# Performance work log

Hardware: AMD Instinct MI355X
Metric: run time of the kernel (lower is better)

## Reference

```python
import jax, jax.numpy as jnp
import numpy as np

B, C = 2, 2
D = H = W = 192
N_BIF = 64                 # bif ids 0..63; labels = bif*4 + stub (stub in 1..3)
NUM_LABELS = 4 * N_BIF     # 256
MIN_STUBS = 2
MIN_VOXELS = 1
TEMP = 0.2


def setup_inputs() -> dict:
    key = jax.random.key(0)
    k1, k2 = jax.random.split(key)
    pred = jax.random.normal(k1, (B, C, D, H, W), dtype=jnp.float32)
    stub_label_map = jax.random.randint(k2, (B, 1, D, H, W), 0, NUM_LABELS).astype(jnp.float32)
    return {"pred": pred, "stub_label_map": stub_label_map}


def reference(pred, stub_label_map):
    # foreground probability: softmax over channel dim, take class 1
    fg = jax.nn.softmax(pred, axis=1)[:, 1]                     # [B,D,H,W]
    labels = jnp.round(stub_label_map[:, 0]).astype(jnp.int32)  # [B,D,H,W]

    Bn = fg.shape[0]
    fg_flat = fg.reshape(Bn, -1)
    lab_flat = labels.reshape(Bn, -1)

    seg = lambda v, i: jax.ops.segment_sum(v, i, num_segments=NUM_LABELS)
    sums = jax.vmap(seg)(fg_flat, lab_flat)                      # [B, NUM_LABELS]
    counts = jax.vmap(seg)(jnp.ones_like(fg_flat), lab_flat)     # [B, NUM_LABELS]

    # group labels as [bif, stub]; drop bif 0 and stub 0 (never used in loop)
    sums = sums.reshape(Bn, N_BIF, 4)[:, 1:, 1:4]                # [B, N_BIF-1, 3]
    counts = counts.reshape(Bn, N_BIF, 4)[:, 1:, 1:4]

    valid = counts >= MIN_VOXELS                                 # stub has enough voxels
    means = sums / jnp.maximum(counts, 1.0)                      # per-stub mean fg prob

    # softmin over the valid stubs of each bif (masked softmax of -mean/temp)
    logits = jnp.where(valid, -means / TEMP, -1e9)
    weights = jax.nn.softmax(logits, axis=-1)
    score = jnp.sum(jnp.where(valid, means * weights, 0.0), axis=-1)  # [B, N_BIF-1]

    valid_bif = jnp.sum(valid, axis=-1) >= MIN_STUBS
    total = jnp.sum(jnp.where(valid_bif, 1.0 - score, 0.0))
    n_bifs = jnp.sum(valid_bif)
    return jnp.where(n_bifs > 0, total / jnp.maximum(n_bifs, 1).astype(total.dtype), 0.0)
```

## Files before the change

kernel.cpp:

```cpp
#include <hip/hip_runtime.h>
#include <math.h>

#define BATCH     2
#define NLAB      256
#define VOX       (192*192*192)
#define TEMP      0.2f
#define GRIDX     768
#define NITER     (VOX / (GRIDX * 1024))
#define NPART     16

#define STEP      4096.0f
#define INV_STEP  (1.0f/4096.0f)

typedef unsigned int u32;
typedef __attribute__((ext_vector_type(8))) short bf16x8;
typedef __attribute__((ext_vector_type(4))) float f32x4;
union FragU { uint4 u; bf16x8 v; };

__device__ __forceinline__ u32 packvox(float pa, float pc, float pl) {
    const float fg = 1.0f / (1.0f + __expf(pa - pc));
    u32 bits = __float_as_uint(fg);
    bits += 0x7FFFu + ((bits >> 16) & 1u);
    const u32 lab = ((u32)(int)(pl + 0.5f)) & 255u;
    return (lab << 24) | (bits >> 16);
}

#define PAIR(de, dodd, aw, b1w, b2w) do {                                   \
    const u32 _e = (de), _o = (dodd);                                       \
    const bool he  = ((_e >> 28) == mlane);                                 \
    const bool ho  = ((_o >> 28) == mlane);                                 \
    const bool le  = (((_e >> 24) & 15u) == mlane);                         \
    const bool lo_ = (((_o >> 24) & 15u) == mlane);                         \
    aw  = (he ? 0x00003F80u : 0u) | (ho  ? 0x3F800000u : 0u);               \
    b1w = (le ? 0x00003F80u : 0u) | (lo_ ? 0x3F800000u : 0u);               \
    b2w = (le ? (_e & 0xFFFFu) : 0u) | (lo_ ? (_o << 16) : 0u);             \
} while (0)

__global__ __launch_bounds__(256, 4) void histo_kernel(
    const float* __restrict__ pred,
    const float* __restrict__ labmap,
    float* __restrict__ ws_slots)
{
    __shared__ __align__(16) u32 s_stage[4][2][256];
    __shared__ float s_cnt[4][NLAB];
    __shared__ float s_sum[4][NLAB];

    const int b    = blockIdx.y;
    const int tid  = threadIdx.x;
    const int w    = tid >> 6;
    const int lane = tid & 63;
    const u32 mlane = (u32)(lane & 15);
    const int g    = lane >> 4;

    const float4* p0 = (const float4*)(pred + (size_t)b * 2 * VOX);
    const float4* p1 = (const float4*)(pred + (size_t)b * 2 * VOX + VOX);
    const float4* lm = (const float4*)(labmap + (size_t)b * VOX);

    f32x4 accC = {0.f, 0.f, 0.f, 0.f};
    f32x4 accS = {0.f, 0.f, 0.f, 0.f};

    const int base = blockIdx.x * 256 + tid;

    #pragma unroll 2
    for (int it = 0; it < NITER; ++it) {
        const int i = base + it * (GRIDX * 256);
        const float4 a = p0[i];
        const float4 c = p1[i];
        const float4 l = lm[i];

        uint4 pkv;
        pkv.x = packvox(a.x, c.x, l.x);
        pkv.y = packvox(a.y, c.y, l.y);
        pkv.z = packvox(a.z, c.z, l.z);
        pkv.w = packvox(a.w, c.w, l.w);

        u32* st = &s_stage[w][it & 1][0];
        *(uint4*)(st + (lane << 2)) = pkv;

        const u32* rp = st + (g << 3);
        #pragma unroll
        for (int t = 0; t < 8; ++t) {
            const uint4 q0 = *(const uint4*)(rp + t * 32);
            const uint4 q1 = *(const uint4*)(rp + t * 32 + 4);
            u32 a0, a1, a2, a3, b10, b11, b12, b13, b20, b21, b22, b23;
            PAIR(q0.x, q0.y, a0, b10, b20);
            PAIR(q0.z, q0.w, a1, b11, b21);
            PAIR(q1.x, q1.y, a2, b12, b22);
            PAIR(q1.z, q1.w, a3, b13, b23);
            FragU A, B1, B2;
            A.u  = make_uint4(a0, a1, a2, a3);
            B1.u = make_uint4(b10, b11, b12, b13);
            B2.u = make_uint4(b20, b21, b22, b23);
            accC = __builtin_amdgcn_mfma_f32_16x16x32_bf16(A.v, B1.v, accC, 0, 0, 0);
            accS = __builtin_amdgcn_mfma_f32_16x16x32_bf16(A.v, B2.v, accS, 0, 0, 0);
        }
    }

    const int row0 = (lane >> 4) << 2;
    const int colb = lane & 15;
    #pragma unroll
    for (int j = 0; j < 4; ++j) {
        s_cnt[w][(row0 + j) * 16 + colb] = accC[j];
        s_sum[w][(row0 + j) * 16 + colb] = accS[j];
    }
    __syncthreads();

    const float cs = s_cnt[0][tid] + s_cnt[1][tid] + s_cnt[2][tid] + s_cnt[3][tid];
    const float ss = s_sum[0][tid] + s_sum[1][tid] + s_sum[2][tid] + s_sum[3][tid];
    ws_slots[((size_t)(b * GRIDX + blockIdx.x)) * NLAB + tid] = ss + STEP * cs;
}

__global__ __launch_bounds__(256) void reduce_kernel(
    const float* __restrict__ ws_slots,
    float* __restrict__ psum,
    float* __restrict__ pcnt)
{
    const int bin  = threadIdx.x;
    const int b    = blockIdx.x / NPART;
    const int part = blockIdx.x % NPART;
    const int per  = GRIDX / NPART;

    float cs = 0.0f, ss = 0.0f;
    for (int s = part * per; s < (part + 1) * per; ++s) {
        float v = ws_slots[((size_t)(b * GRIDX + s)) * NLAB + bin];
        float c = floorf(v * INV_STEP + 0.5f);
        cs += c;
        ss += v - c * STEP;
    }
    psum[(size_t)blockIdx.x * NLAB + bin] = ss;
    pcnt[(size_t)blockIdx.x * NLAB + bin] = cs;
}

__global__ __launch_bounds__(256) void scalar_kernel(
    const float* __restrict__ psum,
    const float* __restrict__ pcnt,
    float* __restrict__ out)
{
    __shared__ float s_fsum[BATCH][NLAB];
    __shared__ float s_fcnt[BATCH][NLAB];

    const int tid = threadIdx.x;

    for (int b = 0; b < BATCH; ++b) {
        float ss = 0.0f, cs = 0.0f;
        for (int p = 0; p < NPART; ++p) {
            ss += psum[(size_t)(b * NPART + p) * NLAB + tid];
            cs += pcnt[(size_t)(b * NPART + p) * NLAB + tid];
        }
        s_fsum[b][tid] = ss;
        s_fcnt[b][tid] = cs;
    }
    __syncthreads();

    if (tid < 64) {
        float total = 0.0f;
        float nbifs = 0.0f;
        if (tid >= 1) {
            for (int bb = 0; bb < BATCH; ++bb) {
                float means[3];
                bool  valid[3];
                int   nvalid = 0;
                for (int s = 0; s < 3; ++s) {
                    int lab = tid * 4 + 1 + s;
                    float cnt = s_fcnt[bb][lab];
                    float sum = s_fsum[bb][lab];
                    valid[s] = (cnt >= 1.0f);
                    means[s] = sum / fmaxf(cnt, 1.0f);
                    nvalid  += valid[s] ? 1 : 0;
                }
                float logits[3], m = -3e38f;
                for (int s = 0; s < 3; ++s) {
                    logits[s] = valid[s] ? (-means[s] / TEMP) : -1e9f;
                    m = fmaxf(m, logits[s]);
                }
                float e[3], se = 0.0f;
                for (int s = 0; s < 3; ++s) { e[s] = __expf(logits[s] - m); se += e[s]; }
                float score = 0.0f;
                for (int s = 0; s < 3; ++s) {
                    if (valid[s]) score += means[s] * (e[s] / se);
                }
                if (nvalid >= 2) {
                    total += 1.0f - score;
                    nbifs += 1.0f;
                }
            }
        }
        for (int off = 32; off > 0; off >>= 1) {
            total += __shfl_down(total, off);
            nbifs += __shfl_down(nbifs, off);
        }
        if (tid == 0) {
            out[0] = (nbifs > 0.0f) ? (total / fmaxf(nbifs, 1.0f)) : 0.0f;
        }
    }
}

extern "C" void kernel_launch(void* const* d_in, const int* in_sizes, int n_in,
                              void* d_out, int out_size, void* d_ws, size_t ws_size,
                              hipStream_t stream) {
    const float* pred = (const float*)d_in[0];
    const float* lab  = (const float*)d_in[1];

    float* ws_slots = (float*)d_ws;
    float* psum = ws_slots + (size_t)BATCH * GRIDX * NLAB;
    float* pcnt = psum + (size_t)BATCH * NPART * NLAB;

    dim3 grid(GRIDX, BATCH);
    histo_kernel<<<grid, 256, 0, stream>>>(pred, lab, ws_slots);
    reduce_kernel<<<BATCH * NPART, 256, 0, stream>>>(ws_slots, psum, pcnt);
    scalar_kernel<<<1, 256, 0, stream>>>(psum, pcnt, (float*)d_out);
}
```

Measured before the change: 217.1 us.

## Split histogram work between LDS-atomic blocks and MFMA blocks in one kernel

The histogram kernel now assigns 4 of every 9 blocks to an LDS-atomic path, which keeps two interleaved histogram copies and skips unused labels. The other 5 of every 9 blocks keep the MFMA one-hot path. Running both paths side by side balances VALU/LDS-atomic work against matrix-core work, and the grid drops to 576 blocks of 12 iterations each with launch bounds relaxed. This adds divergent code paths per block and depends on the two paths covering exactly the whole voxel range. Atomic contention and the fixed 4:5 ratio may not suit the hardware.

Measured after the change: 224.6 us. 3.5% more time.

```diff
diff --git a/kernel.cpp b/kernel.cpp
--- a/kernel.cpp
+++ b/kernel.cpp
@@ -4,10 +4,14 @@
 #define BATCH     2
 #define NLAB      256
 #define VOX       (192*192*192)
+#define VVEC      (VOX/4)
 #define TEMP      0.2f
-#define GRIDX     768
-#define NITER     (VOX / (GRIDX * 1024))
+
+#define BLOCKS    576
+#define NITER     12
 #define NPART     16
+#define NATOMIC_ORDS 256
+#define MFMA_F4_BASE (NATOMIC_ORDS * NITER * 256)
 
 #define STEP      4096.0f
 #define INV_STEP  (1.0f/4096.0f)
@@ -36,78 +40,127 @@
     b2w = (le ? (_e & 0xFFFFu) : 0u) | (lo_ ? (_o << 16) : 0u);             \
 } while (0)
 
-__global__ __launch_bounds__(256, 4) void histo_kernel(
+__global__ __launch_bounds__(256) void histo_kernel(
     const float* __restrict__ pred,
     const float* __restrict__ labmap,
     float* __restrict__ ws_slots)
 {
-    __shared__ __align__(16) u32 s_stage[4][2][256];
-    __shared__ float s_cnt[4][NLAB];
-    __shared__ float s_sum[4][NLAB];
-
-    const int b    = blockIdx.y;
-    const int tid  = threadIdx.x;
-    const int w    = tid >> 6;
-    const int lane = tid & 63;
-    const u32 mlane = (u32)(lane & 15);
-    const int g    = lane >> 4;
+    __shared__ __align__(16) u32 s_lds[4][2][256];
+
+    const int b   = blockIdx.y;
+    const int bx  = blockIdx.x;
+    const int tid = threadIdx.x;
+    const int j   = bx % 9;
+    const int grp = bx / 9;
 
     const float4* p0 = (const float4*)(pred + (size_t)b * 2 * VOX);
     const float4* p1 = (const float4*)(pred + (size_t)b * 2 * VOX + VOX);
     const float4* lm = (const float4*)(labmap + (size_t)b * VOX);
 
-    f32x4 accC = {0.f, 0.f, 0.f, 0.f};
-    f32x4 accS = {0.f, 0.f, 0.f, 0.f};
-
-    const int base = blockIdx.x * 256 + tid;
-
-    #pragma unroll 2
-    for (int it = 0; it < NITER; ++it) {
-        const int i = base + it * (GRIDX * 256);
-        const float4 a = p0[i];
-        const float4 c = p1[i];
-        const float4 l = lm[i];
-
-        uint4 pkv;
-        pkv.x = packvox(a.x, c.x, l.x);
-        pkv.y = packvox(a.y, c.y, l.y);
-        pkv.z = packvox(a.z, c.z, l.z);
-        pkv.w = packvox(a.w, c.w, l.w);
-
-        u32* st = &s_stage[w][it & 1][0];
-        *(uint4*)(st + (lane << 2)) = pkv;
-
-        const u32* rp = st + (g << 3);
+    float val;
+
+    if (j < 4) {
+        float* h = (float*)&s_lds[0][0][0];
+        h[tid] = 0.0f;
+        h[tid + NLAB] = 0.0f;
+        __syncthreads();
+
+        const int ord  = grp * 4 + j;
+        const int copy = (tid & 1) << 8;
+        const int base = ord * (NITER * 256) + tid;
+
+        #pragma unroll 3
+        for (int it = 0; it < NITER; ++it) {
+            const int i = base + it * 256;
+            const float4 a = p0[i];
+            const float4 c = p1[i];
+            const float4 l = lm[i];
+
+            float fg0 = 1.0f / (1.0f + __expf(a.x - c.x));
+            float fg1 = 1.0f / (1.0f + __expf(a.y - c.y));
+            float fg2 = 1.0f / (1.0f + __expf(a.z - c.z));
+            float fg3 = 1.0f / (1.0f + __expf(a.w - c.w));
+
+            int l0 = ((int)(l.x + 0.5f)) & (NLAB - 1);
+            int l1 = ((int)(l.y + 0.5f)) & (NLAB - 1);
+            int l2 = ((int)(l.z + 0.5f)) & (NLAB - 1);
+            int l3 = ((int)(l.w + 0.5f)) & (NLAB - 1);
+
+            if ((l0 & 3) && l0 >= 4) atomicAdd(&h[copy + l0], STEP + fg0);
+            if ((l1 & 3) && l1 >= 4) atomicAdd(&h[copy + l1], STEP + fg1);
+            if ((l2 & 3) && l2 >= 4) atomicAdd(&h[copy + l2], STEP + fg2);
+            if ((l3 & 3) && l3 >= 4) atomicAdd(&h[copy + l3], STEP + fg3);
+        }
+        __syncthreads();
+        val = h[tid] + h[tid + NLAB];
+    } else {
+        const int w    = tid >> 6;
+        const int lane = tid & 63;
+        const u32 mlane = (u32)(lane & 15);
+        const int g    = lane >> 4;
+
+        f32x4 accC = {0.f, 0.f, 0.f, 0.f};
+        f32x4 accS = {0.f, 0.f, 0.f, 0.f};
+
+        const int ord  = grp * 5 + (j - 4);
+        const int base = MFMA_F4_BASE + ord * (NITER * 256) + tid;
+
+        #pragma unroll 2
+        for (int it = 0; it < NITER; ++it) {
+            const int i = base + it * 256;
+            const float4 a = p0[i];
+            const float4 c = p1[i];
+            const float4 l = lm[i];
+
+            uint4 pkv;
+            pkv.x = packvox(a.x, c.x, l.x);
+            pkv.y = packvox(a.y, c.y, l.y);
+            pkv.z = packvox(a.z, c.z, l.z);
+            pkv.w = packvox(a.w, c.w, l.w);
+
+            u32* st = &s_lds[w][it & 1][0];
+            *(uint4*)(st + (lane << 2)) = pkv;
+
+            const u32* rp = st + (g << 3);
+            #pragma unroll
+            for (int t = 0; t < 8; ++t) {
+                const uint4 q0 = *(const uint4*)(rp + t * 32);
+                const uint4 q1 = *(const uint4*)(rp + t * 32 + 4);
+                u32 a0, a1, a2, a3, b10, b11, b12, b13, b20, b21, b22, b23;
+                PAIR(q0.x, q0.y, a0, b10, b20);
+                PAIR(q0.z, q0.w, a1, b11, b21);
+                PAIR(q1.x, q1.y, a2, b12, b22);
+                PAIR(q1.z, q1.w, a3, b13, b23);
+                FragU A, B1, B2;
+                A.u  = make_uint4(a0, a1, a2, a3);
+                B1.u = make_uint4(b10, b11, b12, b13);
+                B2.u = make_uint4(b20, b21, b22, b23);
+                accC = __builtin_amdgcn_mfma_f32_16x16x32_bf16(A.v, B1.v, accC, 0, 0, 0);
+                accS = __builtin_amdgcn_mfma_f32_16x16x32_bf16(A.v, B2.v, accS, 0, 0, 0);
+            }
+        }
+
+        float* cnt_w = (float*)&s_lds[w][0][0];
+        float* sum_w = (float*)&s_lds[w][1][0];
+        const int row0 = (lane >> 4) << 2;
+        const int colb = lane & 15;
         #pragma unroll
-        for (int t = 0; t < 8; ++t) {
-            const uint4 q0 = *(const uint4*)(rp + t * 32);
-            const uint4 q1 = *(const uint4*)(rp + t * 32 + 4);
-            u32 a0, a1, a2, a3, b10, b11, b12, b13, b20, b21, b22, b23;
-            PAIR(q0.x, q0.y, a0, b10, b20);
-            PAIR(q0.z, q0.w, a1, b11, b21);
-            PAIR(q1.x, q1.y, a2, b12, b22);
-            PAIR(q1.z, q1.w, a3, b13, b23);
-            FragU A, B1, B2;
-            A.u  = make_uint4(a0, a1, a2, a3);
-            B1.u = make_uint4(b10, b11, b12, b13);
-            B2.u = make_uint4(b20, b21, b22, b23);
-            accC = __builtin_amdgcn_mfma_f32_16x16x32_bf16(A.v, B1.v, accC, 0, 0, 0);
-            accS = __builtin_amdgcn_mfma_f32_16x16x32_bf16(A.v, B2.v, accS, 0, 0, 0);
-        }
-    }
-
-    const int row0 = (lane >> 4) << 2;
-    const int colb = lane & 15;
-    #pragma unroll
-    for (int j = 0; j < 4; ++j) {
-        s_cnt[w][(row0 + j) * 16 + colb] = accC[j];
-        s_sum[w][(row0 + j) * 16 + colb] = accS[j];
-    }
-    __syncthreads();
-
-    const float cs = s_cnt[0][tid] + s_cnt[1][tid] + s_cnt[2][tid] + s_cnt[3][tid];
-    const float ss = s_sum[0][tid] + s_sum[1][tid] + s_sum[2][tid] + s_sum[3][tid];
-    ws_slots[((size_t)(b * GRIDX + blockIdx.x)) * NLAB + tid] = ss + STEP * cs;
+        for (int jj = 0; jj < 4; ++jj) {
+            cnt_w[(row0 + jj) * 16 + colb] = accC[jj];
+            sum_w[(row0 + jj) * 16 + colb] = accS[jj];
+        }
+        __syncthreads();
+
+        float cs = 0.0f, ss = 0.0f;
+        #pragma unroll
+        for (int ww = 0; ww < 4; ++ww) {
+            cs += ((float*)&s_lds[ww][0][0])[tid];
+            ss += ((float*)&s_lds[ww][1][0])[tid];
+        }
+        val = ss + STEP * cs;
+    }
+
+    ws_slots[((size_t)(b * BLOCKS + bx)) * NLAB + tid] = val;
 }
 
 __global__ __launch_bounds__(256) void reduce_kernel(
@@ -118,11 +171,11 @@
     const int bin  = threadIdx.x;
     const int b    = blockIdx.x / NPART;
     const int part = blockIdx.x % NPART;
-    const int per  = GRIDX / NPART;
+    const int per  = BLOCKS / NPART;
 
     float cs = 0.0f, ss = 0.0f;
     for (int s = part * per; s < (part + 1) * per; ++s) {
-        float v = ws_slots[((size_t)(b * GRIDX + s)) * NLAB + bin];
+        float v = ws_slots[((size_t)(b * BLOCKS + s)) * NLAB + bin];
         float c = floorf(v * INV_STEP + 0.5f);
         cs += c;
         ss += v - c * STEP;
@@ -202,10 +255,10 @@
     const float* lab  = (const float*)d_in[1];
 
     float* ws_slots = (float*)d_ws;
-    float* psum = ws_slots + (size_t)BATCH * GRIDX * NLAB;
+    float* psum = ws_slots + (size_t)BATCH * BLOCKS * NLAB;
     float* pcnt = psum + (size_t)BATCH * NPART * NLAB;
 
-    dim3 grid(GRIDX, BATCH);
+    dim3 grid(BLOCKS, BATCH);
     histo_kernel<<<grid, 256, 0, stream>>>(pred, lab, ws_slots);
     reduce_kernel<<<BATCH * NPART, 256, 0, stream>>>(ws_slots, psum, pcnt);
     scalar_kernel<<<1, 256, 0, stream>>>(psum, pcnt, (float*)d_out);
```
